# Optimization experiments

Measured on AMD Instinct MI355X. Metric: run time of the kernel, lower is better.

## Reference

```python
import jax, jax.numpy as jnp
import numpy as np

N_ITER, K, DIM = 2, 16, 64


def setup_inputs() -> dict:
    key = jax.random.key(0)
    ks = jax.random.split(key, 9)
    B, NE, NU, NR = 8192, 200000, 100000, 32
    return {
        "u": jax.random.randint(ks[0], (B,), 0, NU),
        "v": jax.random.randint(ks[1], (B,), 0, NE),
        "adj_ent": jax.random.randint(ks[2], (NE, K), 0, NE),
        "adj_rel": jax.random.randint(ks[3], (NE, K), 0, NR),
        "usr_emb": jax.random.normal(ks[4], (NU, DIM), jnp.float32) * 0.1,
        "rel_emb": jax.random.normal(ks[5], (NR, DIM), jnp.float32) * 0.1,
        "ent_emb": jax.random.normal(ks[6], (NE, DIM), jnp.float32) * 0.1,
        "W": jax.random.normal(ks[7], (DIM, DIM), jnp.float32) / np.float32(np.sqrt(DIM)),
        "b": jnp.zeros((DIM,), jnp.float32),
    }


def reference(u, v, adj_ent, adj_rel, usr_emb, rel_emb, ent_emb, W, b):
    B = u.shape[0]
    user = usr_emb[u]                                  # [B, D]

    # _get_neighbors: multi-hop fixed-fanout expansion
    entities = [v[:, None]]                            # hop 0: [B, 1]
    relations = []
    for h in range(N_ITER):
        entities.append(adj_ent[entities[h]].reshape(B, -1))   # [B, K^(h+1)]
        relations.append(adj_rel[entities[h]].reshape(B, -1))

    ent_vecs = [ent_emb[e] for e in entities]          # [B, K^h, D] gathers
    rel_vecs = [rel_emb[r] for r in relations]

    # _aggregate: attention-weighted neighbor mix + sum-combine linear
    for i in range(N_ITER):
        act = jnp.tanh if i == N_ITER - 1 else jax.nn.sigmoid
        nxt = []
        for hop in range(N_ITER - i):
            self_v = ent_vecs[hop]                              # [B, m, D]
            neigh = ent_vecs[hop + 1].reshape(B, -1, K, DIM)    # [B, m, K, D]
            rel = rel_vecs[hop].reshape(B, -1, K, DIM)          # [B, m, K, D]
            scores = jnp.einsum('bd,bmkd->bmk', user, rel)      # user-relation
            attn = jax.nn.softmax(scores, axis=-1)              # [B, m, K]
            agg = jnp.einsum('bmk,bmkd->bmd', attn, neigh)      # weighted sum
            nxt.append(act((self_v + agg) @ W + b))             # sum aggregator
        ent_vecs = nxt

    item = ent_vecs[0].reshape(B, DIM)
    return jax.nn.sigmoid(jnp.sum(user * item, axis=1))        # [B]
```

## Files before the change

kernel.cpp:

```cpp
#include <hip/hip_runtime.h>

#define KF    16
#define DIM   64
#define BLOCK 256

typedef __attribute__((ext_vector_type(8))) short bs8;
typedef __attribute__((ext_vector_type(4))) float f32x4;

#define C_FENCE() asm volatile("" ::: "memory")

__device__ __forceinline__ float fsig(float x) {
    return __builtin_amdgcn_rcpf(1.0f + __expf(-x));
}
__device__ __forceinline__ float ftanh(float x) {
    float e = __expf(2.0f * x);
    return 1.0f - 2.0f * __builtin_amdgcn_rcpf(e + 1.0f);
}
__device__ __forceinline__ ushort f2bf(float x) {
    uint u = __builtin_bit_cast(uint, x);
    u += 0x7fffu + ((u >> 16) & 1u);
    return (ushort)(u >> 16);
}
__device__ __forceinline__ float rdlane_f(float v, int l) {
    return __builtin_bit_cast(float, __builtin_amdgcn_readlane(__builtin_bit_cast(int, v), l));
}

__global__ __launch_bounds__(BLOCK) void kgcn_kernel(
    const int* __restrict__ u, const int* __restrict__ v,
    const int* __restrict__ adj_ent, const int* __restrict__ adj_rel,
    const float* __restrict__ usr_emb, const float* __restrict__ rel_emb,
    const float* __restrict__ ent_emb, const float* __restrict__ W,
    const float* __restrict__ bias, float* __restrict__ out, int B)
{
    __shared__ __align__(16) ushort Wfrag[2][4][64][8];
    __shared__ __align__(16) ushort Xl[4][16][72];

    const int tid  = threadIdx.x;
    const int lane = tid & 63;
    const int wv   = tid >> 6;
    const int lr   = lane & 15;
    const int lg   = lane >> 4;

    {
        const int col = wv * 16 + lr;
        bs8 p0, p1;
        #pragma unroll
        for (int i = 0; i < 8; ++i) {
            p0[i] = (short)f2bf(W[(lg * 8 + i) * DIM + col]);
            p1[i] = (short)f2bf(W[(lg * 8 + i + 32) * DIM + col]);
        }
        *(bs8*)&Wfrag[0][wv][lane][0] = p0;
        *(bs8*)&Wfrag[1][wv][lane][0] = p1;
    }
    const float biasr = bias[lane];
    __syncthreads();

    const int   b     = blockIdx.x * 4 + wv;
    const int   e0    = v[b];
    const float user  = usr_emb[(size_t)u[b] * DIM + lane];
    const float ent0v = ent_emb[(size_t)e0 * DIM + lane];

    float ursr;
    {
        const int r  = lane & 31;
        const int hb = lane & 32;
        float s = 0.0f;
        #pragma unroll
        for (int dd = 0; dd < 32; ++dd)
            s = fmaf(__shfl(user, hb + dd), rel_emb[r * DIM + hb + dd], s);
        s += __shfl_xor(s, 32);
        ursr = s;
    }

    int e1r; float at1r;
    {
        e1r = adj_ent[e0 * KF + lr];
        const int r1 = adj_rel[e0 * KF + lr];
        float sc = __shfl(ursr, r1);
        float mx = sc;
        mx = fmaxf(mx, __shfl_xor(mx, 1));
        mx = fmaxf(mx, __shfl_xor(mx, 2));
        mx = fmaxf(mx, __shfl_xor(mx, 4));
        mx = fmaxf(mx, __shfl_xor(mx, 8));
        float e  = __expf(sc - mx);
        float sm = e;
        sm += __shfl_xor(sm, 1);
        sm += __shfl_xor(sm, 2);
        sm += __shfl_xor(sm, 4);
        sm += __shfl_xor(sm, 8);
        at1r = e * __builtin_amdgcn_rcpf(sm);
    }

    int e2r[4]; float at2r[4];
    #pragma unroll
    for (int it = 0; it < 4; ++it) {
        const int m  = it * 4 + lg;
        const int em = __shfl(e1r, m);
        e2r[it] = adj_ent[em * KF + lr];
        const int r2 = adj_rel[em * KF + lr];
        float sc = __shfl(ursr, r2);
        float mx = sc;
        mx = fmaxf(mx, __shfl_xor(mx, 1));
        mx = fmaxf(mx, __shfl_xor(mx, 2));
        mx = fmaxf(mx, __shfl_xor(mx, 4));
        mx = fmaxf(mx, __shfl_xor(mx, 8));
        float e  = __expf(sc - mx);
        float sm = e;
        sm += __shfl_xor(sm, 1);
        sm += __shfl_xor(sm, 2);
        sm += __shfl_xor(sm, 4);
        sm += __shfl_xor(sm, 8);
        at2r[it] = e * __builtin_amdgcn_rcpf(sm);
    }

    float agg0p = 0.0f;
    #pragma unroll
    for (int qo = 0; qo < 4; ++qo) {
        #pragma unroll 1
        for (int qi = 0; qi < 4; ++qi) {
            const int q = qo * 4 + qi;
            float rows[KF + 1];
            #pragma unroll
            for (int k = 0; k < KF; ++k) {
                const int e = __builtin_amdgcn_readlane(e2r[qo], qi * 16 + k);
                rows[k] = ent_emb[(size_t)e * DIM + lane];
            }
            const int es = __builtin_amdgcn_readlane(e1r, q);
            rows[KF] = ent_emb[(size_t)es * DIM + lane];

            float g0 = 0.0f, g1 = 0.0f, g2 = 0.0f, g3 = 0.0f;
            #pragma unroll
            for (int k = 0; k < KF; k += 4) {
                g0 = fmaf(rdlane_f(at2r[qo], qi * 16 + k + 0), rows[k + 0], g0);
                g1 = fmaf(rdlane_f(at2r[qo], qi * 16 + k + 1), rows[k + 1], g1);
                g2 = fmaf(rdlane_f(at2r[qo], qi * 16 + k + 2), rows[k + 2], g2);
                g3 = fmaf(rdlane_f(at2r[qo], qi * 16 + k + 3), rows[k + 3], g3);
            }
            const float selfv = rows[KF];
            agg0p = fmaf(rdlane_f(at1r, q), selfv, agg0p);
            Xl[wv][q][lane] = f2bf(selfv + ((g0 + g1) + (g2 + g3)));
        }
    }
    __syncthreads();

    float bj[4];
    #pragma unroll
    for (int t = 0; t < 4; ++t) bj[t] = __shfl(biasr, t * 16 + lr);

    float agg2r[4];
    {
        const bs8 a0 = *(const bs8*)&Xl[wv][lr][lg * 8];
        const bs8 a1 = *(const bs8*)&Xl[wv][lr][lg * 8 + 32];
        #pragma unroll
        for (int t = 0; t < 4; ++t) {
            f32x4 c; c[0] = bj[t]; c[1] = bj[t]; c[2] = bj[t]; c[3] = bj[t];
            const bs8 w0 = *(const bs8*)&Wfrag[0][t][lane][0];
            const bs8 w1 = *(const bs8*)&Wfrag[1][t][lane][0];
            c = __builtin_amdgcn_mfma_f32_16x16x32_bf16(a0, w0, c, 0, 0, 0);
            c = __builtin_amdgcn_mfma_f32_16x16x32_bf16(a1, w1, c, 0, 0, 0);
            float p = 0.0f;
            #pragma unroll
            for (int r = 0; r < 4; ++r)
                p = fmaf(__shfl(at1r, lg * 4 + r), fsig(c[r]), p);
            p += __shfl_xor(p, 16);
            p += __shfl_xor(p, 32);
            agg2r[t] = p;
        }
    }

    C_FENCE();
    Xl[wv][0][lane] = f2bf(ent0v + agg0p);
    __syncthreads();

    float x2v[4];
    {
        const bs8 a0 = *(const bs8*)&Xl[wv][lr][lg * 8];
        const bs8 a1 = *(const bs8*)&Xl[wv][lr][lg * 8 + 32];
        #pragma unroll
        for (int t = 0; t < 4; ++t) {
            f32x4 c; c[0] = bj[t]; c[1] = bj[t]; c[2] = bj[t]; c[3] = bj[t];
            const bs8 w0 = *(const bs8*)&Wfrag[0][t][lane][0];
            const bs8 w1 = *(const bs8*)&Wfrag[1][t][lane][0];
            c = __builtin_amdgcn_mfma_f32_16x16x32_bf16(a0, w0, c, 0, 0, 0);
            c = __builtin_amdgcn_mfma_f32_16x16x32_bf16(a1, w1, c, 0, 0, 0);
            x2v[t] = fsig(c[0]) + agg2r[t];
        }
    }

    C_FENCE();
    #pragma unroll
    for (int t = 0; t < 4; ++t)
        if (lane < 16) Xl[wv][0][t * 16 + lane] = f2bf(x2v[t]);
    __syncthreads();

    float pv = 0.0f;
    {
        const bs8 a0 = *(const bs8*)&Xl[wv][lr][lg * 8];
        const bs8 a1 = *(const bs8*)&Xl[wv][lr][lg * 8 + 32];
        #pragma unroll
        for (int t = 0; t < 4; ++t) {
            f32x4 c; c[0] = bj[t]; c[1] = bj[t]; c[2] = bj[t]; c[3] = bj[t];
            const bs8 w0 = *(const bs8*)&Wfrag[0][t][lane][0];
            const bs8 w1 = *(const bs8*)&Wfrag[1][t][lane][0];
            c = __builtin_amdgcn_mfma_f32_16x16x32_bf16(a0, w0, c, 0, 0, 0);
            c = __builtin_amdgcn_mfma_f32_16x16x32_bf16(a1, w1, c, 0, 0, 0);
            const float uc = __shfl(user, t * 16 + lr);
            if (lane < 16) pv = fmaf(uc, ftanh(c[0]), pv);
        }
    }
    pv += __shfl_xor(pv, 1);
    pv += __shfl_xor(pv, 2);
    pv += __shfl_xor(pv, 4);
    pv += __shfl_xor(pv, 8);
    if (lane == 0) out[b] = fsig(pv);
}

extern "C" void kernel_launch(void* const* d_in, const int* in_sizes, int n_in,
                              void* d_out, int out_size, void* d_ws, size_t ws_size,
                              hipStream_t stream) {
    const int*   u       = (const int*)d_in[0];
    const int*   v       = (const int*)d_in[1];
    const int*   adj_ent = (const int*)d_in[2];
    const int*   adj_rel = (const int*)d_in[3];
    const float* usr_emb = (const float*)d_in[4];
    const float* rel_emb = (const float*)d_in[5];
    const float* ent_emb = (const float*)d_in[6];
    const float* W       = (const float*)d_in[7];
    const float* bias    = (const float*)d_in[8];
    float* out = (float*)d_out;

    const int B = in_sizes[0];
    kgcn_kernel<<<B / 4, BLOCK, 0, stream>>>(u, v, adj_ent, adj_rel,
                                             usr_emb, rel_emb, ent_emb,
                                             W, bias, out, B);
}
```

Baseline: 193.6 us.

## Double-buffer neighbor row gathers and replace block barriers with wave-local fences

The hop-2 gather loop becomes a fully unrolled software pipeline with two register buffers, so the 17 embedding-row loads for the next neighbor group are issued while the current group is being reduced. The three __syncthreads after writes to each wave's private Xl slice are replaced by compiler fences plus sched_barrier, since the data is only exchanged within one wave. This is meant to hide gather latency and remove block-wide barrier stalls. The cost is higher register pressure from two 17-float buffers, which could lower occupancy. The change also relies on LDS ordering within a wave being correct without an explicit barrier.

```diff
diff --git a/kernel.cpp b/kernel.cpp
--- a/kernel.cpp
+++ b/kernel.cpp
@@ -7,7 +7,8 @@
 typedef __attribute__((ext_vector_type(8))) short bs8;
 typedef __attribute__((ext_vector_type(4))) float f32x4;
 
-#define C_FENCE() asm volatile("" ::: "memory")
+#define C_FENCE() do { asm volatile("" ::: "memory"); \
+                       __builtin_amdgcn_sched_barrier(0); } while (0)
 
 __device__ __forceinline__ float fsig(float x) {
     return __builtin_amdgcn_rcpf(1.0f + __expf(-x));
@@ -114,34 +115,53 @@
     }
 
     float agg0p = 0.0f;
-    #pragma unroll
-    for (int qo = 0; qo < 4; ++qo) {
-        #pragma unroll 1
-        for (int qi = 0; qi < 4; ++qi) {
-            const int q = qo * 4 + qi;
-            float rows[KF + 1];
-            #pragma unroll
-            for (int k = 0; k < KF; ++k) {
-                const int e = __builtin_amdgcn_readlane(e2r[qo], qi * 16 + k);
-                rows[k] = ent_emb[(size_t)e * DIM + lane];
-            }
-            const int es = __builtin_amdgcn_readlane(e1r, q);
-            rows[KF] = ent_emb[(size_t)es * DIM + lane];
-
-            float g0 = 0.0f, g1 = 0.0f, g2 = 0.0f, g3 = 0.0f;
-            #pragma unroll
-            for (int k = 0; k < KF; k += 4) {
-                g0 = fmaf(rdlane_f(at2r[qo], qi * 16 + k + 0), rows[k + 0], g0);
-                g1 = fmaf(rdlane_f(at2r[qo], qi * 16 + k + 1), rows[k + 1], g1);
-                g2 = fmaf(rdlane_f(at2r[qo], qi * 16 + k + 2), rows[k + 2], g2);
-                g3 = fmaf(rdlane_f(at2r[qo], qi * 16 + k + 3), rows[k + 3], g3);
-            }
-            const float selfv = rows[KF];
-            agg0p = fmaf(rdlane_f(at1r, q), selfv, agg0p);
-            Xl[wv][q][lane] = f2bf(selfv + ((g0 + g1) + (g2 + g3)));
-        }
-    }
-    __syncthreads();
+    float bufA[KF + 1], bufB[KF + 1];
+
+#define FETCH(BUF, Q) do {                                                      \
+        _Pragma("unroll")                                                       \
+        for (int k = 0; k < KF; ++k) {                                          \
+            const int e = __builtin_amdgcn_readlane(e2r[(Q) >> 2],              \
+                                                    ((Q) & 3) * 16 + k);        \
+            BUF[k] = ent_emb[(size_t)e * DIM + lane];                           \
+        }                                                                       \
+        BUF[KF] = ent_emb[(size_t)__builtin_amdgcn_readlane(e1r, (Q)) * DIM     \
+                          + lane];                                              \
+    } while (0)
+
+#define CONSUME(BUF, Q) do {                                                    \
+        float g0 = 0.0f, g1 = 0.0f, g2 = 0.0f, g3 = 0.0f;                       \
+        _Pragma("unroll")                                                       \
+        for (int k = 0; k < KF; k += 4) {                                       \
+            g0 = fmaf(rdlane_f(at2r[(Q) >> 2], ((Q) & 3) * 16 + k + 0), BUF[k + 0], g0); \
+            g1 = fmaf(rdlane_f(at2r[(Q) >> 2], ((Q) & 3) * 16 + k + 1), BUF[k + 1], g1); \
+            g2 = fmaf(rdlane_f(at2r[(Q) >> 2], ((Q) & 3) * 16 + k + 2), BUF[k + 2], g2); \
+            g3 = fmaf(rdlane_f(at2r[(Q) >> 2], ((Q) & 3) * 16 + k + 3), BUF[k + 3], g3); \
+        }                                                                       \
+        agg0p = fmaf(rdlane_f(at1r, (Q)), BUF[KF], agg0p);                      \
+        Xl[wv][(Q)][lane] = f2bf(BUF[KF] + ((g0 + g1) + (g2 + g3)));            \
+    } while (0)
+
+    FETCH(bufA, 0);
+    FETCH(bufB, 1);   CONSUME(bufA, 0);
+    FETCH(bufA, 2);   CONSUME(bufB, 1);
+    FETCH(bufB, 3);   CONSUME(bufA, 2);
+    FETCH(bufA, 4);   CONSUME(bufB, 3);
+    FETCH(bufB, 5);   CONSUME(bufA, 4);
+    FETCH(bufA, 6);   CONSUME(bufB, 5);
+    FETCH(bufB, 7);   CONSUME(bufA, 6);
+    FETCH(bufA, 8);   CONSUME(bufB, 7);
+    FETCH(bufB, 9);   CONSUME(bufA, 8);
+    FETCH(bufA, 10);  CONSUME(bufB, 9);
+    FETCH(bufB, 11);  CONSUME(bufA, 10);
+    FETCH(bufA, 12);  CONSUME(bufB, 11);
+    FETCH(bufB, 13);  CONSUME(bufA, 12);
+    FETCH(bufA, 14);  CONSUME(bufB, 13);
+    FETCH(bufB, 15);  CONSUME(bufA, 14);
+    CONSUME(bufB, 15);
+#undef FETCH
+#undef CONSUME
+
+    C_FENCE();
 
     float bj[4];
     #pragma unroll
@@ -170,7 +190,7 @@
 
     C_FENCE();
     Xl[wv][0][lane] = f2bf(ent0v + agg0p);
-    __syncthreads();
+    C_FENCE();
 
     float x2v[4];
     {
@@ -191,7 +211,7 @@
     #pragma unroll
     for (int t = 0; t < 4; ++t)
         if (lane < 16) Xl[wv][0][t * 16 + lane] = f2bf(x2v[t]);
-    __syncthreads();
+    C_FENCE();
 
     float pv = 0.0f;
     {
```

New measurement: 193.0 us. No clear change (-0.3%).

## Split fused KGCN kernel into pre, per-node and tail kernels via workspace

Applied to the files above, without the earlier changes.

Splits the single wave-per-sample kernel into three launches. A prepass computes user-relation scores and hop-1 entities, a per-node kernel gives each hop-1 node its own wave to gather 16 neighbors and write bf16 aggregates to workspace, and a tail kernel does the MFMA layers. This raises parallelism for the latency-bound gather phase (16x more waves) at the cost of extra launches and workspace round-trips. It also replaces intra-wave __syncthreads with compiler fences and sched barriers in both the split tail and the fused fallback, which is used when the workspace is too small.

```diff
diff --git a/kernel.cpp b/kernel.cpp
--- a/kernel.cpp
+++ b/kernel.cpp
@@ -2,12 +2,12 @@
 
 #define KF    16
 #define DIM   64
-#define BLOCK 256
 
 typedef __attribute__((ext_vector_type(8))) short bs8;
 typedef __attribute__((ext_vector_type(4))) float f32x4;
 
-#define C_FENCE() asm volatile("" ::: "memory")
+#define C_FENCE() do { asm volatile("" ::: "memory"); \
+                       __builtin_amdgcn_sched_barrier(0); } while (0)
 
 __device__ __forceinline__ float fsig(float x) {
     return __builtin_amdgcn_rcpf(1.0f + __expf(-x));
@@ -25,7 +25,203 @@
     return __builtin_bit_cast(float, __builtin_amdgcn_readlane(__builtin_bit_cast(int, v), l));
 }
 
-__global__ __launch_bounds__(BLOCK) void kgcn_kernel(
+__device__ __forceinline__ float softmax16(float sc) {
+    float mx = sc;
+    mx = fmaxf(mx, __shfl_xor(mx, 1));
+    mx = fmaxf(mx, __shfl_xor(mx, 2));
+    mx = fmaxf(mx, __shfl_xor(mx, 4));
+    mx = fmaxf(mx, __shfl_xor(mx, 8));
+    float e  = __expf(sc - mx);
+    float sm = e;
+    sm += __shfl_xor(sm, 1);
+    sm += __shfl_xor(sm, 2);
+    sm += __shfl_xor(sm, 4);
+    sm += __shfl_xor(sm, 8);
+    return e * __builtin_amdgcn_rcpf(sm);
+}
+
+__global__ __launch_bounds__(256) void k_pre(
+    const int* __restrict__ u, const int* __restrict__ v,
+    const int* __restrict__ adj_ent,
+    const float* __restrict__ usr_emb, const float* __restrict__ rel_emb,
+    float* __restrict__ urs_ws, int* __restrict__ e1_ws)
+{
+    const int lane = threadIdx.x & 63, wv = threadIdx.x >> 6;
+    const int b  = blockIdx.x * 4 + wv;
+    const int e0 = v[b];
+    const int e1 = adj_ent[e0 * KF + (lane & 15)];
+    const float user = usr_emb[(size_t)u[b] * DIM + lane];
+    const int r = lane & 31, hb = lane & 32;
+    float s = 0.0f;
+    #pragma unroll
+    for (int dd = 0; dd < 32; ++dd)
+        s = fmaf(__shfl(user, hb + dd), rel_emb[r * DIM + hb + dd], s);
+    s += __shfl_xor(s, 32);
+    if (lane < 32) urs_ws[b * 32 + lane] = s;
+    if (lane < KF) e1_ws[b * KF + lane] = e1;
+}
+
+__global__ __launch_bounds__(256) void k_nodes(
+    const int* __restrict__ adj_ent, const int* __restrict__ adj_rel,
+    const float* __restrict__ ent_emb,
+    const float* __restrict__ urs_ws, const int* __restrict__ e1_ws,
+    ushort* __restrict__ Xws)
+{
+    const int lane = threadIdx.x & 63, wv = threadIdx.x >> 6;
+    const int gw = blockIdx.x * 4 + wv;
+    const int b  = gw >> 4;
+    const int lr = lane & 15;
+
+    const int e1m = e1_ws[gw];
+    const int e2v = adj_ent[e1m * KF + lr];
+    const int r2  = adj_rel[e1m * KF + lr];
+    float rows[KF + 1];
+    rows[KF] = ent_emb[(size_t)e1m * DIM + lane];
+    #pragma unroll
+    for (int k = 0; k < KF; ++k) {
+        const int e = __builtin_amdgcn_readlane(e2v, k);
+        rows[k] = ent_emb[(size_t)e * DIM + lane];
+    }
+    const float at2v = softmax16(urs_ws[b * 32 + r2]);
+
+    float g0 = 0.0f, g1 = 0.0f, g2 = 0.0f, g3 = 0.0f;
+    #pragma unroll
+    for (int k = 0; k < KF; k += 4) {
+        g0 = fmaf(rdlane_f(at2v, k + 0), rows[k + 0], g0);
+        g1 = fmaf(rdlane_f(at2v, k + 1), rows[k + 1], g1);
+        g2 = fmaf(rdlane_f(at2v, k + 2), rows[k + 2], g2);
+        g3 = fmaf(rdlane_f(at2v, k + 3), rows[k + 3], g3);
+    }
+    Xws[(size_t)gw * DIM + lane] = f2bf(rows[KF] + ((g0 + g1) + (g2 + g3)));
+}
+
+__global__ __launch_bounds__(256) void k_tail(
+    const int* __restrict__ u, const int* __restrict__ v,
+    const int* __restrict__ adj_rel,
+    const float* __restrict__ usr_emb, const float* __restrict__ ent_emb,
+    const float* __restrict__ W, const float* __restrict__ bias,
+    const float* __restrict__ urs_ws, const int* __restrict__ e1_ws,
+    const ushort* __restrict__ Xws, float* __restrict__ out)
+{
+    __shared__ __align__(16) ushort Wfrag[2][4][64][8];
+    __shared__ __align__(16) ushort Xl[4][16][72];
+
+    const int tid  = threadIdx.x;
+    const int lane = tid & 63;
+    const int wv   = tid >> 6;
+    const int lr   = lane & 15;
+    const int lg   = lane >> 4;
+
+    {
+        const int col = wv * 16 + lr;
+        bs8 p0, p1;
+        #pragma unroll
+        for (int i = 0; i < 8; ++i) {
+            p0[i] = (short)f2bf(W[(lg * 8 + i) * DIM + col]);
+            p1[i] = (short)f2bf(W[(lg * 8 + i + 32) * DIM + col]);
+        }
+        *(bs8*)&Wfrag[0][wv][lane][0] = p0;
+        *(bs8*)&Wfrag[1][wv][lane][0] = p1;
+    }
+    const float biasr = bias[lane];
+    __syncthreads();
+
+    const int   b     = blockIdx.x * 4 + wv;
+    const int   e0    = v[b];
+    const float user  = usr_emb[(size_t)u[b] * DIM + lane];
+    const float ent0v = ent_emb[(size_t)e0 * DIM + lane];
+
+    const int e1r = e1_ws[b * KF + lr];
+    float rows[KF];
+    #pragma unroll
+    for (int k = 0; k < KF; ++k) {
+        const int e = __builtin_amdgcn_readlane(e1r, k);
+        rows[k] = ent_emb[(size_t)e * DIM + lane];
+    }
+    const bs8 a0 = *(const bs8*)&Xws[((size_t)b * KF + lr) * DIM + lg * 8];
+    const bs8 a1 = *(const bs8*)&Xws[((size_t)b * KF + lr) * DIM + lg * 8 + 32];
+
+    const int r1 = adj_rel[e0 * KF + lr];
+    const float at1r = softmax16(urs_ws[b * 32 + r1]);
+
+    float g0 = 0.0f, g1 = 0.0f, g2 = 0.0f, g3 = 0.0f;
+    #pragma unroll
+    for (int k = 0; k < KF; k += 4) {
+        g0 = fmaf(rdlane_f(at1r, k + 0), rows[k + 0], g0);
+        g1 = fmaf(rdlane_f(at1r, k + 1), rows[k + 1], g1);
+        g2 = fmaf(rdlane_f(at1r, k + 2), rows[k + 2], g2);
+        g3 = fmaf(rdlane_f(at1r, k + 3), rows[k + 3], g3);
+    }
+    const float x0 = ent0v + ((g0 + g1) + (g2 + g3));
+
+    float bj[4];
+    #pragma unroll
+    for (int t = 0; t < 4; ++t) bj[t] = __shfl(biasr, t * 16 + lr);
+
+    float agg2r[4];
+    #pragma unroll
+    for (int t = 0; t < 4; ++t) {
+        f32x4 c; c[0] = bj[t]; c[1] = bj[t]; c[2] = bj[t]; c[3] = bj[t];
+        const bs8 w0 = *(const bs8*)&Wfrag[0][t][lane][0];
+        const bs8 w1 = *(const bs8*)&Wfrag[1][t][lane][0];
+        c = __builtin_amdgcn_mfma_f32_16x16x32_bf16(a0, w0, c, 0, 0, 0);
+        c = __builtin_amdgcn_mfma_f32_16x16x32_bf16(a1, w1, c, 0, 0, 0);
+        float p = 0.0f;
+        #pragma unroll
+        for (int r = 0; r < 4; ++r)
+            p = fmaf(__shfl(at1r, lg * 4 + r), fsig(c[r]), p);
+        p += __shfl_xor(p, 16);
+        p += __shfl_xor(p, 32);
+        agg2r[t] = p;
+    }
+
+    Xl[wv][0][lane] = f2bf(x0);
+    C_FENCE();
+
+    float x2v[4];
+    {
+        const bs8 b0 = *(const bs8*)&Xl[wv][lr][lg * 8];
+        const bs8 b1 = *(const bs8*)&Xl[wv][lr][lg * 8 + 32];
+        #pragma unroll
+        for (int t = 0; t < 4; ++t) {
+            f32x4 c; c[0] = bj[t]; c[1] = bj[t]; c[2] = bj[t]; c[3] = bj[t];
+            const bs8 w0 = *(const bs8*)&Wfrag[0][t][lane][0];
+            const bs8 w1 = *(const bs8*)&Wfrag[1][t][lane][0];
+            c = __builtin_amdgcn_mfma_f32_16x16x32_bf16(b0, w0, c, 0, 0, 0);
+            c = __builtin_amdgcn_mfma_f32_16x16x32_bf16(b1, w1, c, 0, 0, 0);
+            x2v[t] = fsig(c[0]) + agg2r[t];
+        }
+    }
+
+    C_FENCE();
+    #pragma unroll
+    for (int t = 0; t < 4; ++t)
+        if (lane < 16) Xl[wv][0][t * 16 + lane] = f2bf(x2v[t]);
+    C_FENCE();
+
+    float pv = 0.0f;
+    {
+        const bs8 b0 = *(const bs8*)&Xl[wv][lr][lg * 8];
+        const bs8 b1 = *(const bs8*)&Xl[wv][lr][lg * 8 + 32];
+        #pragma unroll
+        for (int t = 0; t < 4; ++t) {
+            f32x4 c; c[0] = bj[t]; c[1] = bj[t]; c[2] = bj[t]; c[3] = bj[t];
+            const bs8 w0 = *(const bs8*)&Wfrag[0][t][lane][0];
+            const bs8 w1 = *(const bs8*)&Wfrag[1][t][lane][0];
+            c = __builtin_amdgcn_mfma_f32_16x16x32_bf16(b0, w0, c, 0, 0, 0);
+            c = __builtin_amdgcn_mfma_f32_16x16x32_bf16(b1, w1, c, 0, 0, 0);
+            const float uc = __shfl(user, t * 16 + lr);
+            if (lane < 16) pv = fmaf(uc, ftanh(c[0]), pv);
+        }
+    }
+    pv += __shfl_xor(pv, 1);
+    pv += __shfl_xor(pv, 2);
+    pv += __shfl_xor(pv, 4);
+    pv += __shfl_xor(pv, 8);
+    if (lane == 0) out[b] = fsig(pv);
+}
+
+__global__ __launch_bounds__(256) void kgcn_fused(
     const int* __restrict__ u, const int* __restrict__ v,
     const int* __restrict__ adj_ent, const int* __restrict__ adj_rel,
     const float* __restrict__ usr_emb, const float* __restrict__ rel_emb,
@@ -71,46 +267,18 @@
         s += __shfl_xor(s, 32);
         ursr = s;
     }
-
     int e1r; float at1r;
     {
         e1r = adj_ent[e0 * KF + lr];
-        const int r1 = adj_rel[e0 * KF + lr];
-        float sc = __shfl(ursr, r1);
-        float mx = sc;
-        mx = fmaxf(mx, __shfl_xor(mx, 1));
-        mx = fmaxf(mx, __shfl_xor(mx, 2));
-        mx = fmaxf(mx, __shfl_xor(mx, 4));
-        mx = fmaxf(mx, __shfl_xor(mx, 8));
-        float e  = __expf(sc - mx);
-        float sm = e;
-        sm += __shfl_xor(sm, 1);
-        sm += __shfl_xor(sm, 2);
-        sm += __shfl_xor(sm, 4);
-        sm += __shfl_xor(sm, 8);
-        at1r = e * __builtin_amdgcn_rcpf(sm);
-    }
-
+        at1r = softmax16(__shfl(ursr, adj_rel[e0 * KF + lr]));
+    }
     int e2r[4]; float at2r[4];
     #pragma unroll
     for (int it = 0; it < 4; ++it) {
         const int m  = it * 4 + lg;
         const int em = __shfl(e1r, m);
         e2r[it] = adj_ent[em * KF + lr];
-        const int r2 = adj_rel[em * KF + lr];
-        float sc = __shfl(ursr, r2);
-        float mx = sc;
-        mx = fmaxf(mx, __shfl_xor(mx, 1));
-        mx = fmaxf(mx, __shfl_xor(mx, 2));
-        mx = fmaxf(mx, __shfl_xor(mx, 4));
-        mx = fmaxf(mx, __shfl_xor(mx, 8));
-        float e  = __expf(sc - mx);
-        float sm = e;
-        sm += __shfl_xor(sm, 1);
-        sm += __shfl_xor(sm, 2);
-        sm += __shfl_xor(sm, 4);
-        sm += __shfl_xor(sm, 8);
-        at2r[it] = e * __builtin_amdgcn_rcpf(sm);
+        at2r[it] = softmax16(__shfl(ursr, adj_rel[em * KF + lr]));
     }
 
     float agg0p = 0.0f;
@@ -125,9 +293,7 @@
                 const int e = __builtin_amdgcn_readlane(e2r[qo], qi * 16 + k);
                 rows[k] = ent_emb[(size_t)e * DIM + lane];
             }
-            const int es = __builtin_amdgcn_readlane(e1r, q);
-            rows[KF] = ent_emb[(size_t)es * DIM + lane];
-
+            rows[KF] = ent_emb[(size_t)__builtin_amdgcn_readlane(e1r, q) * DIM + lane];
             float g0 = 0.0f, g1 = 0.0f, g2 = 0.0f, g3 = 0.0f;
             #pragma unroll
             for (int k = 0; k < KF; k += 4) {
@@ -136,12 +302,11 @@
                 g2 = fmaf(rdlane_f(at2r[qo], qi * 16 + k + 2), rows[k + 2], g2);
                 g3 = fmaf(rdlane_f(at2r[qo], qi * 16 + k + 3), rows[k + 3], g3);
             }
-            const float selfv = rows[KF];
-            agg0p = fmaf(rdlane_f(at1r, q), selfv, agg0p);
-            Xl[wv][q][lane] = f2bf(selfv + ((g0 + g1) + (g2 + g3)));
-        }
-    }
-    __syncthreads();
+            agg0p = fmaf(rdlane_f(at1r, q), rows[KF], agg0p);
+            Xl[wv][q][lane] = f2bf(rows[KF] + ((g0 + g1) + (g2 + g3)));
+        }
+    }
+    C_FENCE();
 
     float bj[4];
     #pragma unroll
@@ -167,11 +332,9 @@
             agg2r[t] = p;
         }
     }
-
     C_FENCE();
     Xl[wv][0][lane] = f2bf(ent0v + agg0p);
-    __syncthreads();
-
+    C_FENCE();
     float x2v[4];
     {
         const bs8 a0 = *(const bs8*)&Xl[wv][lr][lg * 8];
@@ -186,13 +349,11 @@
             x2v[t] = fsig(c[0]) + agg2r[t];
         }
     }
-
     C_FENCE();
     #pragma unroll
     for (int t = 0; t < 4; ++t)
         if (lane < 16) Xl[wv][0][t * 16 + lane] = f2bf(x2v[t]);
-    __syncthreads();
-
+    C_FENCE();
     float pv = 0.0f;
     {
         const bs8 a0 = *(const bs8*)&Xl[wv][lr][lg * 8];
@@ -230,7 +391,25 @@
     float* out = (float*)d_out;
 
     const int B = in_sizes[0];
-    kgcn_kernel<<<B / 4, BLOCK, 0, stream>>>(u, v, adj_ent, adj_rel,
-                                             usr_emb, rel_emb, ent_emb,
-                                             W, bias, out, B);
-}
+
+    const size_t off_urs = 0;
+    const size_t off_e1  = off_urs + (size_t)B * 32 * sizeof(float);
+    const size_t off_X   = off_e1  + (size_t)B * KF * sizeof(int);
+    const size_t need    = off_X   + (size_t)B * KF * DIM * sizeof(ushort);
+
+    if (ws_size >= need) {
+        float*  urs_ws = (float*)((char*)d_ws + off_urs);
+        int*    e1_ws  = (int*)  ((char*)d_ws + off_e1);
+        ushort* Xws    = (ushort*)((char*)d_ws + off_X);
+        k_pre  <<<B / 4,          256, 0, stream>>>(u, v, adj_ent, usr_emb, rel_emb,
+                                                    urs_ws, e1_ws);
+        k_nodes<<<(B * KF) / 4,   256, 0, stream>>>(adj_ent, adj_rel, ent_emb,
+                                                    urs_ws, e1_ws, Xws);
+        k_tail <<<B / 4,          256, 0, stream>>>(u, v, adj_rel, usr_emb, ent_emb,
+                                                    W, bias, urs_ws, e1_ws, Xws, out);
+    } else {
+        kgcn_fused<<<B / 4, 256, 0, stream>>>(u, v, adj_ent, adj_rel,
+                                              usr_emb, rel_emb, ent_emb,
+                                              W, bias, out, B);
+    }
+}
```

After: 215.0 us. +11.1%, slower.
